# Kernel tuning notes

Measured on AMD Instinct MI355X. Metric: run time of the kernel, lower is better.

## Reference

```python
import jax, jax.numpy as jnp
import numpy as np

B, LQ, E = 4, 8400, 256
HEADS, LEVELS, POINTS = 8, 4, 4
HEAD_DIM = E // HEADS
SHAPES = [(80, 80), (40, 40), (20, 20), (10, 10)]  # (H, W) per level; sum HW = 8400
LV = sum(h * w for h, w in SHAPES)


def setup_inputs() -> dict:
    key = jax.random.key(0)
    ks = jax.random.split(key, 12)
    query = jax.random.normal(ks[0], (B, LQ, E), jnp.float32)
    # per-level normalized reference points in (0.1, 0.9)
    reference_points = 0.1 + 0.8 * jax.random.uniform(ks[1], (B, LQ, LEVELS, 2), jnp.float32)
    value = jax.random.normal(ks[2], (B, LV, E), jnp.float32)
    spatial_shapes = jnp.array(SHAPES, dtype=jnp.int32)
    s = 0.05
    Wv = jax.random.normal(ks[3], (E, E), jnp.float32) * s
    bv = jnp.zeros((E,), jnp.float32)
    Woff = jax.random.normal(ks[4], (E, HEADS * LEVELS * POINTS * 2), jnp.float32) * 0.01
    boff = jax.random.normal(ks[5], (HEADS * LEVELS * POINTS * 2,), jnp.float32) * 0.02
    Wattn = jax.random.normal(ks[6], (E, HEADS * LEVELS * POINTS), jnp.float32) * s
    battn = jnp.zeros((HEADS * LEVELS * POINTS,), jnp.float32)
    Wo = jax.random.normal(ks[7], (E, E), jnp.float32) * s
    bo = jnp.zeros((E,), jnp.float32)
    return dict(query=query, reference_points=reference_points, value=value,
                spatial_shapes=spatial_shapes, Wv=Wv, bv=bv, Woff=Woff, boff=boff,
                Wattn=Wattn, battn=battn, Wo=Wo, bo=bo)


def _bilinear_sample(vflat, x, y, Hl, Wl):
    # vflat: [BH, D, Hl*Wl]; x, y: [BH, N] pixel coords (align_corners=False convention)
    x0f = jnp.floor(x); y0f = jnp.floor(y)
    wx = (x - x0f)[:, None, :]; wy = (y - y0f)[:, None, :]
    x0 = x0f.astype(jnp.int32); y0 = y0f.astype(jnp.int32)

    def gather(ix, iy):
        valid = ((ix >= 0) & (ix < Wl) & (iy >= 0) & (iy < Hl)).astype(vflat.dtype)
        idx = jnp.clip(iy, 0, Hl - 1) * Wl + jnp.clip(ix, 0, Wl - 1)
        g = jnp.take_along_axis(vflat, idx[:, None, :], axis=2)  # [BH, D, N]
        return g * valid[:, None, :]

    v00 = gather(x0, y0); v01 = gather(x0 + 1, y0)
    v10 = gather(x0, y0 + 1); v11 = gather(x0 + 1, y0 + 1)
    return (v00 * (1 - wx) * (1 - wy) + v01 * wx * (1 - wy)
            + v10 * (1 - wx) * wy + v11 * wx * wy)


def _msda_forward(query, reference_points, value, spatial_shapes,
                  Wv, bv, Woff, boff, Wattn, battn, Wo, bo):
    b, lq, _ = query.shape
    v = (value @ Wv + bv).reshape(b, -1, HEADS, HEAD_DIM)
    off = (query @ Woff + boff).reshape(b, lq, HEADS, LEVELS, POINTS, 2)
    aw = (query @ Wattn + battn).reshape(b, lq, HEADS, LEVELS * POINTS)
    aw = jax.nn.softmax(aw, axis=-1).reshape(b, lq, HEADS, LEVELS, POINTS)
    # normalizer (W, H) per level
    norm = jnp.stack([spatial_shapes[:, 1], spatial_shapes[:, 0]], axis=-1).astype(query.dtype)
    # sampling locations in [0,1]: [B, Lq, H, L, P, 2]
    loc = reference_points[:, :, None, :, None, :] + off / norm[None, None, None, :, None, :]

    sampled_levels = []
    start = 0
    for lvl, (Hl, Wl) in enumerate(SHAPES):
        vl = v[:, start:start + Hl * Wl]                      # [B, Hl*Wl, H, D]
        start += Hl * Wl
        vflat = vl.transpose(0, 2, 3, 1).reshape(b * HEADS, HEAD_DIM, Hl * Wl)
        grid = loc[:, :, :, lvl]                              # [B, Lq, H, P, 2]
        grid = grid.transpose(0, 2, 1, 3, 4).reshape(b * HEADS, lq * POINTS, 2)
        g = grid * 2.0 - 1.0                                  # grid_sample convention
        x = (g[..., 0] + 1.0) * (Wl * 0.5) - 0.5
        y = (g[..., 1] + 1.0) * (Hl * 0.5) - 0.5
        s = _bilinear_sample(vflat, x, y, Hl, Wl)             # [BH, D, Lq*P]
        sampled_levels.append(s.reshape(b, HEADS, HEAD_DIM, lq, POINTS))
    sampled = jnp.stack(sampled_levels, axis=-1)              # [B, H, D, Lq, P, L]
    out = jnp.einsum('bhdqpl,bqhlp->bqhd', sampled, aw).reshape(b, lq, E)
    return out @ Wo + bo


def reference(query, reference_points, value, spatial_shapes,
              Wv, bv, Woff, boff, Wattn, battn, Wo, bo):
    return _msda_forward(query, reference_points, value, spatial_shapes,
                         Wv, bv, Woff, boff, Wattn, battn, Wo, bo)
```

## Files before the change

### kernel.cpp

```cpp
#include <hip/hip_runtime.h>
#include <math.h>

#define BB 4
#define LQ 8400
#define NH 8
#define LVTOT 8500
#define HD 32

typedef __attribute__((ext_vector_type(8))) short short8;
typedef __attribute__((ext_vector_type(4))) float f32x4;
typedef __attribute__((ext_vector_type(2))) float f32x2;
typedef unsigned short ushort_t;

__device__ __forceinline__ ushort_t f2bf(float f) {
    union { float f; unsigned u; } v; v.f = f;
    unsigned r = v.u + 0x7fffu + ((v.u >> 16) & 1u);
    return (ushort_t)(r >> 16);
}
__device__ __forceinline__ float bflo(unsigned u) {
    union { unsigned u; float f; } x; x.u = u << 16; return x.f;
}
__device__ __forceinline__ float bfhi(unsigned u) {
    union { unsigned u; float f; } x; x.u = u & 0xffff0000u; return x.f;
}
__device__ __forceinline__ f32x2 up2(unsigned u) {
    return (f32x2){bflo(u), bfhi(u)};
}

__device__ __forceinline__ void dma16(const ushort_t* g, ushort_t* l) {
    __builtin_amdgcn_global_load_lds(
        (const __attribute__((address_space(1))) void*)g,
        (__attribute__((address_space(3))) void*)l, 16, 0, 0);
}

__global__ __launch_bounds__(256) void prep_all(
    const float* __restrict__ value, const float* __restrict__ query,
    const float* __restrict__ Wv, const float* __restrict__ Woff,
    const float* __restrict__ Wattn, const float* __restrict__ Wo,
    ushort_t* __restrict__ value_b, ushort_t* __restrict__ query_b,
    ushort_t* __restrict__ BT)
{
    const int bid = blockIdx.x;
    if (bid < 16900) {
        const float* src = (bid < 8500) ? value : query;
        ushort_t* dst = (bid < 8500) ? value_b : query_b;
        int i = (bid < 8500 ? bid : bid - 8500) * 256 + threadIdx.x;
        float4 f = ((const float4*)src)[i];
        ushort4 o;
        o.x = f2bf(f.x); o.y = f2bf(f.y); o.z = f2bf(f.z); o.w = f2bf(f.w);
        ((ushort4*)dst)[i] = o;
    } else {
        int idx = (bid - 16900) * 256 + threadIdx.x;
        int r = idx >> 8, k = idx & 255;
        float v;
        if (r < 256) v = Wv[k * 256 + r];
        else if (r < 640) {
            int n = r - 256;
            v = (n < 256) ? Woff[k * 256 + n] : Wattn[k * 128 + (n - 256)];
        } else v = Wo[k * 256 + (r - 640)];
        BT[idx] = f2bf(v);
    }
}

__device__ __forceinline__ void gemm_core(
    const ushort_t* __restrict__ A, const ushort_t* __restrict__ B, int M,
    int m0, int n0, ushort_t* Asl, ushort_t* Bsl, f32x4 acc[4][4])
{
    const int tid  = threadIdx.x;
    const int wave = tid >> 6, lane = tid & 63;
    const int quad = lane >> 4, mr = lane & 15;
    const int wm   = (wave >> 1) * 64, wn = (wave & 1) * 64;
    const int oct  = lane >> 3;
    const int bseg = lane & 7;

    for (int k0 = 0; k0 < 256; k0 += 64) {
        __syncthreads();
        #pragma unroll
        for (int i = 0; i < 4; i++) {
            int m  = i * 32 + wave * 8 + oct;
            int gs = bseg ^ (m & 7);
            int am = min(m0 + m, M - 1);
            dma16(A + (size_t)am * 256 + k0 + gs * 8,
                  Asl + (size_t)(i * 32 + wave * 8) * 64 + lane * 8);
            int bn = n0 + m;
            dma16(B + (size_t)bn * 256 + k0 + gs * 8,
                  Bsl + (size_t)(i * 32 + wave * 8) * 64 + lane * 8);
        }
        __syncthreads();
        #pragma unroll
        for (int ks = 0; ks < 2; ks++) {
            short8 af[4], bf[4];
            const int ksl = ks * 4 + quad;
            #pragma unroll
            for (int i = 0; i < 4; i++) {
                int m = wm + i * 16 + mr;
                af[i] = *(const short8*)&Asl[m * 64 + (ksl ^ (m & 7)) * 8];
                int n = wn + i * 16 + mr;
                bf[i] = *(const short8*)&Bsl[n * 64 + (ksl ^ (n & 7)) * 8];
            }
            #pragma unroll
            for (int i = 0; i < 4; i++)
                #pragma unroll
                for (int j = 0; j < 4; j++)
                    acc[i][j] = __builtin_amdgcn_mfma_f32_16x16x32_bf16(
                        af[i], bf[j], acc[i][j], 0, 0, 0);
        }
    }
}

__global__ __launch_bounds__(256, 3) void gemm_fused(
    const ushort_t* __restrict__ Av, const ushort_t* __restrict__ Aq,
    const ushort_t* __restrict__ BT,
    const float* __restrict__ bv, const float* __restrict__ boff,
    const float* __restrict__ battn,
    ushort_t* __restrict__ vperm, ushort_t* __restrict__ off_b,
    ushort_t* __restrict__ awl_b)
{
    __shared__ ushort_t Asl[128 * 64];
    __shared__ ushort_t Bsl[128 * 64];

    const int bid = blockIdx.x;
    int mode, m0, n0, M;
    const ushort_t *A, *B;
    if (bid < 532) { mode = 0; m0 = (bid % 266) * 128; n0 = (bid / 266) * 128;
                     A = Av; B = BT; M = 34000; }
    else { int b2 = bid - 532;
           mode = 1; m0 = (b2 % 263) * 128; n0 = (b2 / 263) * 128;
           A = Aq; B = BT + 65536; M = 33600; }

    f32x4 acc[4][4];
    #pragma unroll
    for (int i = 0; i < 4; i++)
        #pragma unroll
        for (int j = 0; j < 4; j++) acc[i][j] = (f32x4){0.f, 0.f, 0.f, 0.f};

    gemm_core(A, B, M, m0, n0, Asl, Bsl, acc);

    const int tid  = threadIdx.x;
    const int wave = tid >> 6, lane = tid & 63;
    const int quad = lane >> 4, mr = lane & 15;
    const int wm   = (wave >> 1) * 64, wn = (wave & 1) * 64;

    #pragma unroll
    for (int i = 0; i < 4; i++) {
        const int rbase = m0 + wm + i * 16 + quad * 4;
        #pragma unroll
        for (int j = 0; j < 4; j++) {
            const int c = n0 + wn + j * 16 + mr;
            #pragma unroll
            for (int reg = 0; reg < 4; reg++) {
                int row = rbase + reg;
                if (row >= M) continue;
                float val = acc[i][j][reg];
                if (mode == 0) {
                    float o = val + bv[c];
                    int b = row / LVTOT, pix = row - b * LVTOT;
                    int h = c >> 5, d = c & 31;
                    vperm[(((size_t)(b * NH + h)) * LVTOT + pix) * HD + d] = f2bf(o);
                } else {
                    if (c < 256) off_b[(size_t)row * 256 + c] = f2bf(val + boff[c]);
                    else awl_b[(size_t)row * 128 + (c - 256)] = f2bf(val + battn[c - 256]);
                }
            }
        }
    }
}

__global__ __launch_bounds__(256, 3) void gemm_out(
    const ushort_t* __restrict__ A, const ushort_t* __restrict__ BT,
    const float* __restrict__ bo, float* __restrict__ out)
{
    __shared__ ushort_t Asl[128 * 64];
    __shared__ ushort_t Bsl[128 * 64];

    const int m0 = (blockIdx.x % 263) * 128;
    const int n0 = (blockIdx.x / 263) * 128;
    const int M = 33600;

    f32x4 acc[4][4];
    #pragma unroll
    for (int i = 0; i < 4; i++)
        #pragma unroll
        for (int j = 0; j < 4; j++) acc[i][j] = (f32x4){0.f, 0.f, 0.f, 0.f};

    gemm_core(A, BT, M, m0, n0, Asl, Bsl, acc);

    const int tid  = threadIdx.x;
    const int wave = tid >> 6, lane = tid & 63;
    const int quad = lane >> 4, mr = lane & 15;
    const int wm   = (wave >> 1) * 64, wn = (wave & 1) * 64;

    #pragma unroll
    for (int i = 0; i < 4; i++) {
        const int rbase = m0 + wm + i * 16 + quad * 4;
        #pragma unroll
        for (int j = 0; j < 4; j++) {
            const int c = n0 + wn + j * 16 + mr;
            #pragma unroll
            for (int reg = 0; reg < 4; reg++) {
                int row = rbase + reg;
                if (row >= M) continue;
                out[(size_t)row * 256 + c] = acc[i][j][reg] + bo[c];
            }
        }
    }
}

__global__ __launch_bounds__(256) void msda_sample(
    const ushort_t* __restrict__ vperm, const ushort_t* __restrict__ off,
    const ushort_t* __restrict__ awl, const float* __restrict__ refp,
    ushort_t* __restrict__ sampled)
{
    __shared__ float4 s_w[16 * 33];
    __shared__ int4   s_i[16 * 33];

    const int tid = threadIdx.x;
    const int bid = blockIdx.x;
    const int h   = bid & 7;
    const int r   = bid >> 3;
    const int b   = r / 263;
    const int c   = r - b * 263;
    const int q0b = c * 32;
    const int bq0 = b * LQ + q0b;

    const int Hs[4]   = {80, 40, 20, 10};
    const int base[4] = {0, 6400, 8000, 8400};

    #pragma unroll
    for (int it = 0; it < 2; it++) {
        const int s  = it * 256 + tid;
        const int ql = s >> 4, lp = s & 15;
        const int l  = lp >> 2;
        const int qv = (q0b + ql < LQ) ? ql : 0;
        const size_t bq = (size_t)(bq0 + qv);
        const int Wl = Hs[l];

        unsigned od = *(const unsigned*)(off + bq * 256 + h * 32 + lp * 2);
        float ox = bflo(od), oy = bfhi(od);
        float lgt = bflo((unsigned)awl[bq * 128 + h * 16 + lp]);
        float e = __expf(lgt);
        float sum = e;
        sum += __shfl_xor(sum, 1, 16);
        sum += __shfl_xor(sum, 2, 16);
        sum += __shfl_xor(sum, 4, 16);
        sum += __shfl_xor(sum, 8, 16);
        float aw = e * __builtin_amdgcn_rcpf(sum);

        float2 rp = *(const float2*)(refp + bq * 8 + l * 2);
        float x = rp.x * (float)Wl + ox - 0.5f;
        float y = rp.y * (float)Wl + oy - 0.5f;
        float x0f = floorf(x), y0f = floorf(y);
        float wx = x - x0f, wy = y - y0f;
        int x0 = (int)x0f, y0 = (int)y0f;
        bool vx0 = (x0 >= 0) & (x0 < Wl);
        bool vx1 = (x0 + 1 >= 0) & (x0 + 1 < Wl);
        bool vy0 = (y0 >= 0) & (y0 < Wl);
        bool vy1 = (y0 + 1 >= 0) & (y0 + 1 < Wl);
        int cx0 = min(max(x0, 0), Wl - 1);
        int cx1 = min(max(x0 + 1, 0), Wl - 1);
        int cy0 = min(max(y0, 0), Wl - 1);
        int cy1 = min(max(y0 + 1, 0), Wl - 1);
        float w00 = (vx0 && vy0) ? (1.f - wx) * (1.f - wy) * aw : 0.f;
        float w01 = (vx1 && vy0) ? wx * (1.f - wy) * aw : 0.f;
        float w10 = (vx0 && vy1) ? (1.f - wx) * wy * aw : 0.f;
        float w11 = (vx1 && vy1) ? wx * wy * aw : 0.f;
        const int rec = lp * 33 + ql;
        s_w[rec] = make_float4(w00, w01, w10, w11);
        s_i[rec] = make_int4((base[l] + cy0 * Wl + cx0) << 6,
                             (base[l] + cy0 * Wl + cx1) << 6,
                             (base[l] + cy1 * Wl + cx0) << 6,
                             (base[l] + cy1 * Wl + cx1) << 6);
    }
    __syncthreads();

    const int ql  = tid >> 3;
    const int l8  = tid & 7;
    const int dby = l8 * 8;

    if (q0b + ql < LQ) {
        const char* plane = (const char*)(vperm + (size_t)(b * NH + h) * (LVTOT * HD));
        f32x2 a01 = (f32x2){0.f, 0.f};
        f32x2 a23 = (f32x2){0.f, 0.f};
        #pragma unroll
        for (int pt = 0; pt < 16; pt++) {
            const int rec = pt * 33 + ql;
            float4 w  = s_w[rec];
            int4   iv = s_i[rec];
            uint2 v0 = *(const uint2*)(plane + (unsigned)(iv.x + dby));
            uint2 v1 = *(const uint2*)(plane + (unsigned)(iv.y + dby));
            uint2 v2 = *(const uint2*)(plane + (unsigned)(iv.z + dby));
            uint2 v3 = *(const uint2*)(plane + (unsigned)(iv.w + dby));
            f32x2 wx2 = (f32x2){w.x, w.x};
            f32x2 wy2 = (f32x2){w.y, w.y};
            f32x2 wz2 = (f32x2){w.z, w.z};
            f32x2 ww2 = (f32x2){w.w, w.w};
            a01 = __builtin_elementwise_fma(wx2, up2(v0.x), a01);
            a01 = __builtin_elementwise_fma(wy2, up2(v1.x), a01);
            a01 = __builtin_elementwise_fma(wz2, up2(v2.x), a01);
            a01 = __builtin_elementwise_fma(ww2, up2(v3.x), a01);
            a23 = __builtin_elementwise_fma(wx2, up2(v0.y), a23);
            a23 = __builtin_elementwise_fma(wy2, up2(v1.y), a23);
            a23 = __builtin_elementwise_fma(wz2, up2(v2.y), a23);
            a23 = __builtin_elementwise_fma(ww2, up2(v3.y), a23);
        }
        const size_t bq = (size_t)(bq0 + ql);
        ushort4 o;
        o.x = f2bf(a01[0]); o.y = f2bf(a01[1]);
        o.z = f2bf(a23[0]); o.w = f2bf(a23[1]);
        *(ushort4*)(sampled + bq * 256 + h * 32 + l8 * 4) = o;
    }
}

extern "C" void kernel_launch(void* const* d_in, const int* in_sizes, int n_in,
                              void* d_out, int out_size, void* d_ws, size_t ws_size,
                              hipStream_t stream) {
    const float* query = (const float*)d_in[0];
    const float* refp  = (const float*)d_in[1];
    const float* value = (const float*)d_in[2];
    const float* Wv    = (const float*)d_in[4];
    const float* bv    = (const float*)d_in[5];
    const float* Woff  = (const float*)d_in[6];
    const float* boff  = (const float*)d_in[7];
    const float* Wattn = (const float*)d_in[8];
    const float* battn = (const float*)d_in[9];
    const float* Wo    = (const float*)d_in[10];
    const float* bo    = (const float*)d_in[11];
    float* out = (float*)d_out;

    ushort_t* ws = (ushort_t*)d_ws;
    ushort_t* off_b   = ws;
    ushort_t* awl_b   = off_b + 8601600;
    ushort_t* value_b = awl_b + 4300800;
    ushort_t* query_b = value_b + 8704000;
    ushort_t* vperm_b = query_b + 8601600;
    ushort_t* BT      = vperm_b + 8704000;
    ushort_t* sampled_b = query_b;

    prep_all<<<dim3(17796), 256, 0, stream>>>(
        value, query, Wv, Woff, Wattn, Wo, value_b, query_b, BT);

    gemm_fused<<<dim3(532 + 789), 256, 0, stream>>>(
        value_b, query_b, BT, bv, boff, battn, vperm_b, off_b, awl_b);

    msda_sample<<<dim3(8 * 4 * 263), 256, 0, stream>>>(
        vperm_b, off_b, awl_b, refp, sampled_b);

    gemm_out<<<dim3(526), 256, 0, stream>>>(
        sampled_b, BT + 163840, bo, out);
}
```

Measured before the change: 248.3 us.

## Store projected values as fp16 and use packed fdot2 in sampler with batched gathers

The value projection now writes fp16 instead of bf16, and the bilinear weights are packed to fp16 pairs in shared memory. The sampler then combines corner pairs with v_perm and accumulates through fdot2 instructions, with gathers batched four points at a time to raise memory-level parallelism. GEMM block index mapping is also changed so that adjacent blocks share the same M tile across N tiles, which should improve L2 reuse of A. The fp16 value storage is a precision change that could overflow or lose range compared with bf16. Weights rounded toward zero to fp16 also add some error.

```diff
diff --git a/kernel.cpp b/kernel.cpp
--- a/kernel.cpp
+++ b/kernel.cpp
@@ -10,6 +10,8 @@
 typedef __attribute__((ext_vector_type(8))) short short8;
 typedef __attribute__((ext_vector_type(4))) float f32x4;
 typedef __attribute__((ext_vector_type(2))) float f32x2;
+typedef __attribute__((ext_vector_type(2))) _Float16 half2_t;
+typedef __attribute__((ext_vector_type(2))) __fp16 fp16x2_t;
 typedef unsigned short ushort_t;
 
 __device__ __forceinline__ ushort_t f2bf(float f) {
@@ -23,8 +25,11 @@
 __device__ __forceinline__ float bfhi(unsigned u) {
     union { unsigned u; float f; } x; x.u = u & 0xffff0000u; return x.f;
 }
-__device__ __forceinline__ f32x2 up2(unsigned u) {
-    return (f32x2){bflo(u), bfhi(u)};
+__device__ __forceinline__ half2_t ash2(unsigned u) {
+    union { unsigned u; half2_t h; } x; x.u = u; return x.h;
+}
+__device__ __forceinline__ unsigned pk2u(fp16x2_t h) {
+    union { fp16x2_t h; unsigned u; } x; x.h = h; return x.u;
 }
 
 __device__ __forceinline__ void dma16(const ushort_t* g, ushort_t* l) {
@@ -122,10 +127,10 @@
     const int bid = blockIdx.x;
     int mode, m0, n0, M;
     const ushort_t *A, *B;
-    if (bid < 532) { mode = 0; m0 = (bid % 266) * 128; n0 = (bid / 266) * 128;
+    if (bid < 532) { mode = 0; m0 = (bid >> 1) * 128; n0 = (bid & 1) * 128;
                      A = Av; B = BT; M = 34000; }
     else { int b2 = bid - 532;
-           mode = 1; m0 = (b2 % 263) * 128; n0 = (b2 / 263) * 128;
+           mode = 1; m0 = (b2 / 3) * 128; n0 = (b2 % 3) * 128;
            A = Aq; B = BT + 65536; M = 33600; }
 
     f32x4 acc[4][4];
@@ -156,7 +161,9 @@
                     float o = val + bv[c];
                     int b = row / LVTOT, pix = row - b * LVTOT;
                     int h = c >> 5, d = c & 31;
-                    vperm[(((size_t)(b * NH + h)) * LVTOT + pix) * HD + d] = f2bf(o);
+                    union { _Float16 h16; ushort_t u; } cv;
+                    cv.h16 = (_Float16)o;
+                    vperm[(((size_t)(b * NH + h)) * LVTOT + pix) * HD + d] = cv.u;
                 } else {
                     if (c < 256) off_b[(size_t)row * 256 + c] = f2bf(val + boff[c]);
                     else awl_b[(size_t)row * 128 + (c - 256)] = f2bf(val + battn[c - 256]);
@@ -173,8 +180,8 @@
     __shared__ ushort_t Asl[128 * 64];
     __shared__ ushort_t Bsl[128 * 64];
 
-    const int m0 = (blockIdx.x % 263) * 128;
-    const int n0 = (blockIdx.x / 263) * 128;
+    const int m0 = (blockIdx.x >> 1) * 128;
+    const int n0 = (blockIdx.x & 1) * 128;
     const int M = 33600;
 
     f32x4 acc[4][4];
@@ -211,8 +218,8 @@
     const ushort_t* __restrict__ awl, const float* __restrict__ refp,
     ushort_t* __restrict__ sampled)
 {
-    __shared__ float4 s_w[16 * 33];
-    __shared__ int4   s_i[16 * 33];
+    __shared__ uint2 s_w[16 * 33];
+    __shared__ int4  s_i[16 * 33];
 
     const int tid = threadIdx.x;
     const int bid = blockIdx.x;
@@ -265,7 +272,8 @@
         float w10 = (vx0 && vy1) ? (1.f - wx) * wy * aw : 0.f;
         float w11 = (vx1 && vy1) ? wx * wy * aw : 0.f;
         const int rec = lp * 33 + ql;
-        s_w[rec] = make_float4(w00, w01, w10, w11);
+        s_w[rec] = make_uint2(pk2u(__builtin_amdgcn_cvt_pkrtz(w00, w01)),
+                              pk2u(__builtin_amdgcn_cvt_pkrtz(w10, w11)));
         s_i[rec] = make_int4((base[l] + cy0 * Wl + cx0) << 6,
                              (base[l] + cy0 * Wl + cx1) << 6,
                              (base[l] + cy1 * Wl + cx0) << 6,
@@ -279,34 +287,50 @@
 
     if (q0b + ql < LQ) {
         const char* plane = (const char*)(vperm + (size_t)(b * NH + h) * (LVTOT * HD));
-        f32x2 a01 = (f32x2){0.f, 0.f};
-        f32x2 a23 = (f32x2){0.f, 0.f};
-        #pragma unroll
-        for (int pt = 0; pt < 16; pt++) {
-            const int rec = pt * 33 + ql;
-            float4 w  = s_w[rec];
-            int4   iv = s_i[rec];
-            uint2 v0 = *(const uint2*)(plane + (unsigned)(iv.x + dby));
-            uint2 v1 = *(const uint2*)(plane + (unsigned)(iv.y + dby));
-            uint2 v2 = *(const uint2*)(plane + (unsigned)(iv.z + dby));
-            uint2 v3 = *(const uint2*)(plane + (unsigned)(iv.w + dby));
-            f32x2 wx2 = (f32x2){w.x, w.x};
-            f32x2 wy2 = (f32x2){w.y, w.y};
-            f32x2 wz2 = (f32x2){w.z, w.z};
-            f32x2 ww2 = (f32x2){w.w, w.w};
-            a01 = __builtin_elementwise_fma(wx2, up2(v0.x), a01);
-            a01 = __builtin_elementwise_fma(wy2, up2(v1.x), a01);
-            a01 = __builtin_elementwise_fma(wz2, up2(v2.x), a01);
-            a01 = __builtin_elementwise_fma(ww2, up2(v3.x), a01);
-            a23 = __builtin_elementwise_fma(wx2, up2(v0.y), a23);
-            a23 = __builtin_elementwise_fma(wy2, up2(v1.y), a23);
-            a23 = __builtin_elementwise_fma(wz2, up2(v2.y), a23);
-            a23 = __builtin_elementwise_fma(ww2, up2(v3.y), a23);
+        float a0 = 0.f, a1 = 0.f, a2 = 0.f, a3 = 0.f;
+        #pragma unroll
+        for (int pg = 0; pg < 4; pg++) {
+            uint2 wv[4]; int4 iv[4];
+            #pragma unroll
+            for (int t = 0; t < 4; t++) {
+                const int rec = (pg * 4 + t) * 33 + ql;
+                wv[t] = s_w[rec];
+                iv[t] = s_i[rec];
+            }
+            uint2 g0[4], g1[4], g2[4], g3[4];
+            #pragma unroll
+            for (int t = 0; t < 4; t++) {
+                g0[t] = *(const uint2*)(plane + (unsigned)(iv[t].x + dby));
+                g1[t] = *(const uint2*)(plane + (unsigned)(iv[t].y + dby));
+                g2[t] = *(const uint2*)(plane + (unsigned)(iv[t].z + dby));
+                g3[t] = *(const uint2*)(plane + (unsigned)(iv[t].w + dby));
+            }
+            #pragma unroll
+            for (int t = 0; t < 4; t++) {
+                half2_t w01 = ash2(wv[t].x);
+                half2_t w23 = ash2(wv[t].y);
+                unsigned p01lo = __builtin_amdgcn_perm(g1[t].x, g0[t].x, 0x05040100);
+                unsigned p01hi = __builtin_amdgcn_perm(g1[t].x, g0[t].x, 0x07060302);
+                unsigned p23lo = __builtin_amdgcn_perm(g3[t].x, g2[t].x, 0x05040100);
+                unsigned p23hi = __builtin_amdgcn_perm(g3[t].x, g2[t].x, 0x07060302);
+                a0 = __builtin_amdgcn_fdot2(w01, ash2(p01lo), a0, false);
+                a0 = __builtin_amdgcn_fdot2(w23, ash2(p23lo), a0, false);
+                a1 = __builtin_amdgcn_fdot2(w01, ash2(p01hi), a1, false);
+                a1 = __builtin_amdgcn_fdot2(w23, ash2(p23hi), a1, false);
+                unsigned q01lo = __builtin_amdgcn_perm(g1[t].y, g0[t].y, 0x05040100);
+                unsigned q01hi = __builtin_amdgcn_perm(g1[t].y, g0[t].y, 0x07060302);
+                unsigned q23lo = __builtin_amdgcn_perm(g3[t].y, g2[t].y, 0x05040100);
+                unsigned q23hi = __builtin_amdgcn_perm(g3[t].y, g2[t].y, 0x07060302);
+                a2 = __builtin_amdgcn_fdot2(w01, ash2(q01lo), a2, false);
+                a2 = __builtin_amdgcn_fdot2(w23, ash2(q23lo), a2, false);
+                a3 = __builtin_amdgcn_fdot2(w01, ash2(q01hi), a3, false);
+                a3 = __builtin_amdgcn_fdot2(w23, ash2(q23hi), a3, false);
+            }
         }
         const size_t bq = (size_t)(bq0 + ql);
         ushort4 o;
-        o.x = f2bf(a01[0]); o.y = f2bf(a01[1]);
-        o.z = f2bf(a23[0]); o.w = f2bf(a23[1]);
+        o.x = f2bf(a0); o.y = f2bf(a1);
+        o.z = f2bf(a2); o.w = f2bf(a3);
         *(ushort4*)(sampled + bq * 256 + h * 32 + l8 * 4) = o;
     }
 }
```

Result: no change. 248.1 us (-0.1%).
